# Kernel tuning notes

Measured on AMD Instinct MI355X. Metric: run time of the kernel, lower is better.

## Reference

```python
import jax, jax.numpy as jnp
import numpy as np

B, T, IN_DIM, OUT_DIM = 1024, 64, 8, 2
H, K, HIDDEN = 3, 5, 256
LOG_STD_MIN, LOG_STD_MAX = -20.0, 2.0


def setup_inputs() -> dict:
    key = jax.random.key(0)
    ks = jax.random.split(key, 12)
    def lin(k, fan_in, fan_out):
        b = 1.0 / np.sqrt(fan_in)
        return jax.random.uniform(k, (fan_in, fan_out), jnp.float32, -b, b)
    inp = {
        'state': jax.random.normal(ks[0], (B, T, IN_DIM), jnp.float32),
        'noise': jax.random.normal(ks[1], (B, T, OUT_DIM), jnp.float32),
        'Wq': lin(ks[2], IN_DIM, K * H),
        'Wk': lin(ks[3], K, K * H),
        'Wv': lin(ks[4], K, K * H),
        'W1': lin(ks[5], K * H + IN_DIM, HIDDEN),
        'b1': jnp.zeros((HIDDEN,), jnp.float32),
        'W2': lin(ks[6], HIDDEN, HIDDEN),
        'b2': jnp.zeros((HIDDEN,), jnp.float32),
        'Wmu': jax.random.uniform(ks[7], (HIDDEN, OUT_DIM), jnp.float32, -0.003, 0.003),
        'bmu': jax.random.uniform(ks[8], (OUT_DIM,), jnp.float32, -0.003, 0.003),
        'Wls': jax.random.uniform(ks[9], (HIDDEN, OUT_DIM), jnp.float32, -0.003, 0.003),
        'bls': jax.random.uniform(ks[10], (OUT_DIM,), jnp.float32, -0.003, 0.003),
    }
    return inp


# static off-diagonal neighbor indices: row i -> all j != i
_OFFDIAG = np.array([[j for j in range(T) if j != i] for i in range(T)], dtype=np.int32)


def _forward(state, noise, Wq, Wk, Wv, W1, b1, W2, b2, Wmu, bmu, Wls, bls):
    b, t, _ = state.shape
    # rel[b,i,j] = state[b,j,:4] - state[b,i,:4]
    rel4 = state[:, None, :, 0:4] - state[:, :, None, 0:4]          # [b,t,t,4] (x,y,vx,vy)
    x_comp = rel4[..., 0::2]                                         # [x, vx]
    y_comp = rel4[..., 1::2]                                         # [y, vy]
    ang = (-state[:, :, 7] + 0.5 * jnp.pi)[:, None, :, None]         # varies with j (own-ref of key agent)
    c, s = jnp.cos(ang), jnp.sin(ang)
    xn = x_comp * c - y_comp * s                                     # [x', vx']
    yn = x_comp * s + y_comp * c                                     # [y', vy']
    rel = jnp.stack([xn[..., 0], yn[..., 0], xn[..., 1], yn[..., 1]], axis=-1)  # [b,t,t,4]
    # drop self-pairs (diagonal) -> [b,t,t-1,4]
    idx = jnp.asarray(_OFFDIAG)
    rel_od = rel[:, jnp.arange(t)[:, None], idx]
    r = jnp.sqrt(rel_od[..., 0] ** 2 + rel_od[..., 1] ** 2)[..., None]   # [b,t,t-1,1]
    r_trans = jax.nn.sigmoid(1.0 - 5.0 * (r - 0.2))                       # 1/(1+exp(-1+5(r-0.2)))
    rel_n = jnp.concatenate([rel_od[..., 0:2] / r, rel_od[..., 2:4], r_trans], axis=-1)  # [b,t,t-1,5]
    h, k = H, K
    q = (state @ Wq).reshape(b, t, h, k)                              # [b,t,h,k]
    keys = (rel_n @ Wk).reshape(b, t, t - 1, h, k)                    # [b,t,n,h,k]
    vals = (rel_n @ Wv).reshape(b, t, t - 1, h, k)
    scores = jnp.einsum('btnhk,bthk->bthn', keys, q) / jnp.sqrt(jnp.float32(k))
    w = jax.nn.softmax(scores, axis=-1)                               # over t-1 neighbors
    att = jnp.einsum('bthn,btnhk->bthk', w, vals).reshape(b, t, h * k)
    x = jnp.concatenate([att, state], axis=-1)
    x = jax.nn.relu(x @ W1 + b1)
    x = jax.nn.relu(x @ W2 + b2)
    mu = jnp.tanh(x @ Wmu + bmu)
    log_std = jnp.tanh(x @ Wls + bls)
    log_std = LOG_STD_MIN + 0.5 * (LOG_STD_MAX - LOG_STD_MIN) * (log_std + 1.0)
    std = jnp.exp(log_std)
    z = mu + std * noise                                              # rsample with explicit noise
    action = jnp.tanh(z)
    # Normal(mu,std).log_prob(z) with (z-mu)/std == noise
    log_prob = -0.5 * noise ** 2 - log_std - 0.5 * jnp.log(2.0 * jnp.pi)
    log_prob = log_prob - jnp.log(1.0 - action ** 2 + 1e-7)
    log_prob = jnp.sum(log_prob, axis=-1, keepdims=True)
    return action, log_prob


def reference(state, noise, Wq, Wk, Wv, W1, b1, W2, b2, Wmu, bmu, Wls, bls):
    return _forward(state, noise, Wq, Wk, Wv, W1, b1, W2, b2, Wmu, bmu, Wls, bls)
```

## Files before the change

kernel.cpp:

```cpp
#include <hip/hip_runtime.h>
#include <math.h>

#define NROWS 65536

typedef short bf16x8 __attribute__((ext_vector_type(8)));
typedef float f32x4  __attribute__((ext_vector_type(4)));

__device__ __forceinline__ unsigned short f2bf(float x){
    unsigned int u = __float_as_uint(x);
    u += 0x7FFFu + ((u >> 16) & 1u);
    return (unsigned short)(u >> 16);
}

template<int CTRL, int RM>
__device__ __forceinline__ float dpp_add(float v){
    int m = __builtin_amdgcn_update_dpp(0, __float_as_int(v), CTRL, RM, 0xF, 1);
    return v + __int_as_float(m);
}
__device__ __forceinline__ float rowsum16(float v){
    v = dpp_add<0x111, 0xF>(v);
    v = dpp_add<0x112, 0xF>(v);
    v = dpp_add<0x114, 0xF>(v);
    v = dpp_add<0x118, 0xF>(v);
    return v;
}
__device__ __forceinline__ float bfly8_add(float v){
    v = dpp_add<0xB1, 0xF>(v);
    v = dpp_add<0x4E, 0xF>(v);
    v = dpp_add<0x141, 0xF>(v);
    return v;
}

__global__ __launch_bounds__(256) void prep_kernel(
    const float* __restrict__ W2, const float* __restrict__ W1,
    unsigned short* __restrict__ w2frag, unsigned short* __restrict__ w1frag)
{
    const int bx = blockIdx.x, t = threadIdx.x;
    if (bx < 128){
        const int ct = bx >> 3, kk = bx & 7;
        #pragma unroll
        for (int s = 0; s < 2; ++s){
            int f = t * 2 + s;
            int lane = f >> 3, e = f & 7;
            int k = kk * 32 + (lane >> 4) * 8 + e;
            int c = ct * 16 + (lane & 15);
            w2frag[(size_t)(ct * 8 + kk) * 512 + f] = f2bf(W2[k * 256 + c]);
        }
    } else {
        #pragma unroll
        for (int s = 0; s < 32; ++s){
            int flat = t * 32 + s;
            int ct = flat >> 9, r = flat & 511;
            int lane = r >> 3, e = r & 7;
            int k = (lane >> 4) * 8 + e;
            int c = ct * 16 + (lane & 15);
            w1frag[flat] = (k < 23) ? f2bf(W1[k * 256 + c]) : (unsigned short)0;
        }
    }
}

__global__ __launch_bounds__(512, 4) void actor_kernel(
    const float* __restrict__ state, const float* __restrict__ noise,
    const float* __restrict__ Wq, const float* __restrict__ Wk,
    const float* __restrict__ Wv,
    const unsigned short* __restrict__ w1frag, const float* __restrict__ b1,
    const unsigned short* __restrict__ w2frag, const float* __restrict__ b2,
    const float* __restrict__ Wmu, const float* __restrict__ bmu,
    const float* __restrict__ Wls, const float* __restrict__ bls,
    float* __restrict__ action_out, float* __restrict__ logprob_out)
{
    __shared__ __align__(16) unsigned char uniA[64 * 264 * 2];
    float* sLDS  = (float*)uniA;
    float* pjLDS = sLDS + 576;
    float* qkLDS = pjLDS + 512;
    unsigned short* h1LDS = (unsigned short*)uniA;
    __shared__ __align__(16) unsigned short x0LDS[64 * 40];
    __shared__ float headLDS[8 * 64 * 5];

    const int t    = threadIdx.x;
    const int lane = t & 63;
    const int w    = t >> 6;
    const int lm   = lane & 15;
    const int lq   = lane >> 4;
    const int b    = blockIdx.x;

    {
        float v = state[(size_t)b * 512 + t];
        int r = t >> 3, c = t & 7;
        sLDS[r * 9 + c] = v;
        if (c < 4) pjLDS[r * 8 + c] = v;
    }
    __syncthreads();

    if (t < 192){
        const int row = t & 63, h = t >> 6;
        float s[8];
        #pragma unroll
        for (int d = 0; d < 8; ++d) s[d] = sLDS[row * 9 + d];
        float q[5];
        #pragma unroll
        for (int e = 0; e < 5; ++e){
            int m = h * 5 + e;
            float acc = 0.f;
            #pragma unroll
            for (int d = 0; d < 8; ++d) acc += s[d] * Wq[d * 15 + m];
            q[e] = acc;
        }
        #pragma unroll
        for (int f = 0; f < 5; ++f){
            float acc = 0.f;
            #pragma unroll
            for (int kk = 0; kk < 5; ++kk) acc += Wk[f * 15 + h * 5 + kk] * q[kk];
            qkLDS[row * 17 + h * 5 + f] = acc * 0.64519834f;
        }
    } else if (w == 7){
        const int row = lane;
        float ang = 1.5707963267948966f - sLDS[row * 9 + 7];
        float sn, cs;
        __sincosf(ang, &sn, &cs);
        pjLDS[row * 8 + 4] = sn;
        pjLDS[row * 8 + 5] = cs;
    }
    __syncthreads();

    {
        const int il = lane >> 3;
        const int js = lane & 7;
        const int i  = w * 8 + il;
        const float si0 = sLDS[i * 9 + 0], si1 = sLDS[i * 9 + 1];
        const float si2 = sLDS[i * 9 + 2], si3 = sLDS[i * 9 + 3];
        float qkv[15];
        #pragma unroll
        for (int m = 0; m < 15; ++m) qkv[m] = qkLDS[i * 17 + m];

        float s0 = 0.f, s1 = 0.f, s2 = 0.f;
        float g0[5] = {0,0,0,0,0}, g1[5] = {0,0,0,0,0}, g2[5] = {0,0,0,0,0};
        #pragma unroll
        for (int jj = 0; jj < 8; ++jj){
            const int j = jj * 8 + js;
            float4 pj = *(const float4*)&pjLDS[j * 8];
            float sn = pjLDS[j * 8 + 4], cs = pjLDS[j * 8 + 5];
            float d0 = pj.x - si0, d1 = pj.y - si1, d2 = pj.z - si2, d3 = pj.w - si3;
            float xn0 = d0 * cs - d1 * sn, yn0 = d0 * sn + d1 * cs;
            float xn1 = d2 * cs - d3 * sn, yn1 = d2 * sn + d3 * cs;
            float r2v = xn0 * xn0 + yn0 * yn0;
            bool self = (j == i);
            float inv_r = self ? 0.f : rsqrtf(r2v);
            float rv = r2v * inv_r;
            float ex = exp2f(rv * 7.2134752f - 2.8853901f);
            float f4 = 1.f / (1.f + ex);
            float f0 = xn0 * inv_r, f1 = yn0 * inv_r;
            float sc0 = f0*qkv[0]  + f1*qkv[1]  + xn1*qkv[2]  + yn1*qkv[3]  + f4*qkv[4];
            float sc1 = f0*qkv[5]  + f1*qkv[6]  + xn1*qkv[7]  + yn1*qkv[8]  + f4*qkv[9];
            float sc2 = f0*qkv[10] + f1*qkv[11] + xn1*qkv[12] + yn1*qkv[13] + f4*qkv[14];
            float e0 = self ? 0.f : exp2f(sc0);
            float e1 = self ? 0.f : exp2f(sc1);
            float e2 = self ? 0.f : exp2f(sc2);
            s0 += e0; s1 += e1; s2 += e2;
            g0[0] += e0*f0; g0[1] += e0*f1; g0[2] += e0*xn1; g0[3] += e0*yn1; g0[4] += e0*f4;
            g1[0] += e1*f0; g1[1] += e1*f1; g1[2] += e1*xn1; g1[3] += e1*yn1; g1[4] += e1*f4;
            g2[0] += e2*f0; g2[1] += e2*f1; g2[2] += e2*xn1; g2[3] += e2*yn1; g2[4] += e2*f4;
        }
        s0 = bfly8_add(s0); s1 = bfly8_add(s1); s2 = bfly8_add(s2);
        #pragma unroll
        for (int f = 0; f < 5; ++f){
            g0[f] = bfly8_add(g0[f]);
            g1[f] = bfly8_add(g1[f]);
            g2[f] = bfly8_add(g2[f]);
        }
        float i0 = 1.f / s0, i1 = 1.f / s1, i2 = 1.f / s2;

        #pragma unroll
        for (int mm = 0; mm < 2; ++mm){
            int m = js * 2 + mm;
            if (m < 15){
                float G0 = (m < 5) ? g0[0] : (m < 10) ? g1[0] : g2[0];
                float G1 = (m < 5) ? g0[1] : (m < 10) ? g1[1] : g2[1];
                float G2 = (m < 5) ? g0[2] : (m < 10) ? g1[2] : g2[2];
                float G3 = (m < 5) ? g0[3] : (m < 10) ? g1[3] : g2[3];
                float G4 = (m < 5) ? g0[4] : (m < 10) ? g1[4] : g2[4];
                float I  = (m < 5) ? i0    : (m < 10) ? i1    : i2;
                float av = (G0 * Wv[m] + G1 * Wv[15 + m] + G2 * Wv[30 + m]
                          + G3 * Wv[45 + m] + G4 * Wv[60 + m]) * I;
                x0LDS[i * 40 + m] = f2bf(av);
            }
        }
        x0LDS[i * 40 + 15 + js] = f2bf(sLDS[i * 9 + js]);
        x0LDS[i * 40 + 23 + js] = 0;
        if (js == 0) x0LDS[i * 40 + 31] = 0;
    }
    __syncthreads();

    {
        bf16x8 afr[4];
        #pragma unroll
        for (int rt = 0; rt < 4; ++rt)
            afr[rt] = *(const bf16x8*)&x0LDS[(rt * 16 + lm) * 40 + lq * 8];
        #pragma unroll
        for (int ci = 0; ci < 2; ++ci){
            const int ct = w * 2 + ci;
            bf16x8 bfr = *(const bf16x8*)&w1frag[(size_t)ct * 512 + lane * 8];
            float bb = b1[ct * 16 + lm];
            #pragma unroll
            for (int rt = 0; rt < 4; ++rt){
                f32x4 c0 = {0.f, 0.f, 0.f, 0.f};
                c0 = __builtin_amdgcn_mfma_f32_16x16x32_bf16(afr[rt], bfr, c0, 0, 0, 0);
                #pragma unroll
                for (int p = 0; p < 4; ++p)
                    h1LDS[(rt * 16 + lq * 4 + p) * 264 + ct * 16 + lm] = f2bf(fmaxf(c0[p] + bb, 0.f));
            }
        }
    }
    __syncthreads();

    {
        f32x4 acc[4][2];
        #pragma unroll
        for (int rt = 0; rt < 4; ++rt)
            #pragma unroll
            for (int ci = 0; ci < 2; ++ci) acc[rt][ci] = (f32x4){0.f, 0.f, 0.f, 0.f};

        #pragma unroll
        for (int kk = 0; kk < 8; ++kk){
            bf16x8 arf[4], brf[2];
            #pragma unroll
            for (int rt = 0; rt < 4; ++rt)
                arf[rt] = *(const bf16x8*)&h1LDS[(rt * 16 + lm) * 264 + kk * 32 + lq * 8];
            #pragma unroll
            for (int ci = 0; ci < 2; ++ci)
                brf[ci] = *(const bf16x8*)&w2frag[(size_t)((w * 2 + ci) * 8 + kk) * 512 + lane * 8];
            #pragma unroll
            for (int rt = 0; rt < 4; ++rt)
                #pragma unroll
                for (int ci = 0; ci < 2; ++ci)
                    acc[rt][ci] = __builtin_amdgcn_mfma_f32_16x16x32_bf16(arf[rt], brf[ci], acc[rt][ci], 0, 0, 0);
        }

        float bb[2];
        float2 wm[2], wl[2];
        #pragma unroll
        for (int ci = 0; ci < 2; ++ci){
            int c = (w * 2 + ci) * 16 + lm;
            bb[ci] = b2[c];
            wm[ci] = *(const float2*)&Wmu[c * 2];
            wl[ci] = *(const float2*)&Wls[c * 2];
        }
        #pragma unroll
        for (int rt = 0; rt < 4; ++rt){
            #pragma unroll
            for (int p = 0; p < 4; ++p){
                float m0 = 0.f, m1 = 0.f, l0 = 0.f, l1 = 0.f;
                #pragma unroll
                for (int ci = 0; ci < 2; ++ci){
                    float hv = fmaxf(acc[rt][ci][p] + bb[ci], 0.f);
                    m0 += hv * wm[ci].x;
                    m1 += hv * wm[ci].y;
                    l0 += hv * wl[ci].x;
                    l1 += hv * wl[ci].y;
                }
                m0 = rowsum16(m0); m1 = rowsum16(m1);
                l0 = rowsum16(l0); l1 = rowsum16(l1);
                if (lm == 15){
                    int row = rt * 16 + lq * 4 + p;
                    float* hp = &headLDS[(w * 64 + row) * 5];
                    hp[0] = m0; hp[1] = m1; hp[2] = l0; hp[3] = l1;
                }
            }
        }
    }
    __syncthreads();

    if (t < 64){
        const int row = t;
        float m0 = 0.f, m1 = 0.f, l0 = 0.f, l1 = 0.f;
        #pragma unroll
        for (int ww = 0; ww < 8; ++ww){
            const float* hp = &headLDS[(ww * 64 + row) * 5];
            m0 += hp[0]; m1 += hp[1]; l0 += hp[2]; l1 += hp[3];
        }
        const size_t grow = (size_t)b * 64 + row;
        float n0 = noise[grow * 2 + 0];
        float n1 = noise[grow * 2 + 1];
        float lp = 0.f;
        {
            float mu = tanhf(m0 + bmu[0]);
            float ls = tanhf(l0 + bls[0]);
            ls = -20.f + 11.f * (ls + 1.f);
            float sd = expf(ls);
            float a = tanhf(mu + sd * n0);
            action_out[grow * 2 + 0] = a;
            lp += -0.5f * n0 * n0 - ls - 0.9189385332046727f - logf(1.f - a * a + 1e-7f);
        }
        {
            float mu = tanhf(m1 + bmu[1]);
            float ls = tanhf(l1 + bls[1]);
            ls = -20.f + 11.f * (ls + 1.f);
            float sd = expf(ls);
            float a = tanhf(mu + sd * n1);
            action_out[grow * 2 + 1] = a;
            lp += -0.5f * n1 * n1 - ls - 0.9189385332046727f - logf(1.f - a * a + 1e-7f);
        }
        logprob_out[grow] = lp;
    }
}

extern "C" void kernel_launch(void* const* d_in, const int* in_sizes, int n_in,
                              void* d_out, int out_size, void* d_ws, size_t ws_size,
                              hipStream_t stream)
{
    (void)in_sizes; (void)n_in; (void)out_size; (void)ws_size;
    const float* state = (const float*)d_in[0];
    const float* noise = (const float*)d_in[1];
    const float* Wq  = (const float*)d_in[2];
    const float* Wk  = (const float*)d_in[3];
    const float* Wv  = (const float*)d_in[4];
    const float* W1  = (const float*)d_in[5];
    const float* b1  = (const float*)d_in[6];
    const float* W2  = (const float*)d_in[7];
    const float* b2  = (const float*)d_in[8];
    const float* Wmu = (const float*)d_in[9];
    const float* bmu = (const float*)d_in[10];
    const float* Wls = (const float*)d_in[11];
    const float* bls = (const float*)d_in[12];

    unsigned short* w2frag = (unsigned short*)d_ws;
    unsigned short* w1frag = w2frag + 65536;

    float* action_out  = (float*)d_out;
    float* logprob_out = (float*)d_out + (size_t)NROWS * 2;

    prep_kernel<<<129, 256, 0, stream>>>(W2, W1, w2frag, w1frag);
    actor_kernel<<<1024, 512, 0, stream>>>(state, noise, Wq, Wk, Wv,
        w1frag, b1, w2frag, b2, Wmu, bmu, Wls, bls, action_out, logprob_out);
}
```

Baseline: 122.1 us.

## Split each batch element across two 256-thread blocks of 32 query rows

```diff
diff --git a/kernel.cpp b/kernel.cpp
--- a/kernel.cpp
+++ b/kernel.cpp
@@ -59,7 +59,7 @@
     }
 }
 
-__global__ __launch_bounds__(512, 4) void actor_kernel(
+__global__ __launch_bounds__(256, 6) void actor_kernel(
     const float* __restrict__ state, const float* __restrict__ noise,
     const float* __restrict__ Wq, const float* __restrict__ Wk,
     const float* __restrict__ Wv,
@@ -69,31 +69,35 @@
     const float* __restrict__ Wls, const float* __restrict__ bls,
     float* __restrict__ action_out, float* __restrict__ logprob_out)
 {
-    __shared__ __align__(16) unsigned char uniA[64 * 264 * 2];
+    __shared__ __align__(16) unsigned char uniA[32 * 264 * 2];
     float* sLDS  = (float*)uniA;
     float* pjLDS = sLDS + 576;
     float* qkLDS = pjLDS + 512;
     unsigned short* h1LDS = (unsigned short*)uniA;
-    __shared__ __align__(16) unsigned short x0LDS[64 * 40];
-    __shared__ float headLDS[8 * 64 * 5];
-
-    const int t    = threadIdx.x;
-    const int lane = t & 63;
-    const int w    = t >> 6;
-    const int lm   = lane & 15;
-    const int lq   = lane >> 4;
-    const int b    = blockIdx.x;
-
-    {
-        float v = state[(size_t)b * 512 + t];
-        int r = t >> 3, c = t & 7;
+    __shared__ __align__(16) unsigned short x0LDS[32 * 40];
+    __shared__ float headLDS[4 * 32 * 5];
+
+    const int t     = threadIdx.x;
+    const int lane  = t & 63;
+    const int w     = t >> 6;
+    const int lm    = lane & 15;
+    const int lq    = lane >> 4;
+    const int b     = blockIdx.x >> 1;
+    const int ibase = (blockIdx.x & 1) * 32;
+
+    #pragma unroll
+    for (int s = 0; s < 2; ++s){
+        int idx = t + s * 256;
+        float v = state[(size_t)b * 512 + idx];
+        int r = idx >> 3, c = idx & 7;
         sLDS[r * 9 + c] = v;
         if (c < 4) pjLDS[r * 8 + c] = v;
     }
     __syncthreads();
 
-    if (t < 192){
-        const int row = t & 63, h = t >> 6;
+    if (t < 96){
+        const int rloc = t & 31, h = t >> 5;
+        const int row = ibase + rloc;
         float s[8];
         #pragma unroll
         for (int d = 0; d < 8; ++d) s[d] = sLDS[row * 9 + d];
@@ -111,10 +115,10 @@
             float acc = 0.f;
             #pragma unroll
             for (int kk = 0; kk < 5; ++kk) acc += Wk[f * 15 + h * 5 + kk] * q[kk];
-            qkLDS[row * 17 + h * 5 + f] = acc * 0.64519834f;
-        }
-    } else if (w == 7){
-        const int row = lane;
+            qkLDS[rloc * 17 + h * 5 + f] = acc * 0.64519834f;
+        }
+    } else if (t < 160){
+        const int row = t - 96;
         float ang = 1.5707963267948966f - sLDS[row * 9 + 7];
         float sn, cs;
         __sincosf(ang, &sn, &cs);
@@ -126,12 +130,13 @@
     {
         const int il = lane >> 3;
         const int js = lane & 7;
-        const int i  = w * 8 + il;
+        const int iloc = w * 8 + il;
+        const int i = ibase + iloc;
         const float si0 = sLDS[i * 9 + 0], si1 = sLDS[i * 9 + 1];
         const float si2 = sLDS[i * 9 + 2], si3 = sLDS[i * 9 + 3];
         float qkv[15];
         #pragma unroll
-        for (int m = 0; m < 15; ++m) qkv[m] = qkLDS[i * 17 + m];
+        for (int m = 0; m < 15; ++m) qkv[m] = qkLDS[iloc * 17 + m];
 
         float s0 = 0.f, s1 = 0.f, s2 = 0.f;
         float g0[5] = {0,0,0,0,0}, g1[5] = {0,0,0,0,0}, g2[5] = {0,0,0,0,0};
@@ -182,27 +187,27 @@
                 float I  = (m < 5) ? i0    : (m < 10) ? i1    : i2;
                 float av = (G0 * Wv[m] + G1 * Wv[15 + m] + G2 * Wv[30 + m]
                           + G3 * Wv[45 + m] + G4 * Wv[60 + m]) * I;
-                x0LDS[i * 40 + m] = f2bf(av);
+                x0LDS[iloc * 40 + m] = f2bf(av);
             }
         }
-        x0LDS[i * 40 + 15 + js] = f2bf(sLDS[i * 9 + js]);
-        x0LDS[i * 40 + 23 + js] = 0;
-        if (js == 0) x0LDS[i * 40 + 31] = 0;
+        x0LDS[iloc * 40 + 15 + js] = f2bf(sLDS[i * 9 + js]);
+        x0LDS[iloc * 40 + 23 + js] = 0;
+        if (js == 0) x0LDS[iloc * 40 + 31] = 0;
     }
     __syncthreads();
 
     {
-        bf16x8 afr[4];
-        #pragma unroll
-        for (int rt = 0; rt < 4; ++rt)
+        bf16x8 afr[2];
+        #pragma unroll
+        for (int rt = 0; rt < 2; ++rt)
             afr[rt] = *(const bf16x8*)&x0LDS[(rt * 16 + lm) * 40 + lq * 8];
         #pragma unroll
-        for (int ci = 0; ci < 2; ++ci){
-            const int ct = w * 2 + ci;
+        for (int ci = 0; ci < 4; ++ci){
+            const int ct = w * 4 + ci;
             bf16x8 bfr = *(const bf16x8*)&w1frag[(size_t)ct * 512 + lane * 8];
             float bb = b1[ct * 16 + lm];
             #pragma unroll
-            for (int rt = 0; rt < 4; ++rt){
+            for (int rt = 0; rt < 2; ++rt){
                 f32x4 c0 = {0.f, 0.f, 0.f, 0.f};
                 c0 = __builtin_amdgcn_mfma_f32_16x16x32_bf16(afr[rt], bfr, c0, 0, 0, 0);
                 #pragma unroll
@@ -214,44 +219,44 @@
     __syncthreads();
 
     {
-        f32x4 acc[4][2];
-        #pragma unroll
-        for (int rt = 0; rt < 4; ++rt)
-            #pragma unroll
-            for (int ci = 0; ci < 2; ++ci) acc[rt][ci] = (f32x4){0.f, 0.f, 0.f, 0.f};
+        f32x4 acc[2][4];
+        #pragma unroll
+        for (int rt = 0; rt < 2; ++rt)
+            #pragma unroll
+            for (int ci = 0; ci < 4; ++ci) acc[rt][ci] = (f32x4){0.f, 0.f, 0.f, 0.f};
 
         #pragma unroll
         for (int kk = 0; kk < 8; ++kk){
-            bf16x8 arf[4], brf[2];
-            #pragma unroll
-            for (int rt = 0; rt < 4; ++rt)
+            bf16x8 arf[2], brf[4];
+            #pragma unroll
+            for (int rt = 0; rt < 2; ++rt)
                 arf[rt] = *(const bf16x8*)&h1LDS[(rt * 16 + lm) * 264 + kk * 32 + lq * 8];
             #pragma unroll
-            for (int ci = 0; ci < 2; ++ci)
-                brf[ci] = *(const bf16x8*)&w2frag[(size_t)((w * 2 + ci) * 8 + kk) * 512 + lane * 8];
-            #pragma unroll
-            for (int rt = 0; rt < 4; ++rt)
+            for (int ci = 0; ci < 4; ++ci)
+                brf[ci] = *(const bf16x8*)&w2frag[(size_t)((w * 4 + ci) * 8 + kk) * 512 + lane * 8];
+            #pragma unroll
+            for (int rt = 0; rt < 2; ++rt)
                 #pragma unroll
-                for (int ci = 0; ci < 2; ++ci)
+                for (int ci = 0; ci < 4; ++ci)
                     acc[rt][ci] = __builtin_amdgcn_mfma_f32_16x16x32_bf16(arf[rt], brf[ci], acc[rt][ci], 0, 0, 0);
         }
 
-        float bb[2];
-        float2 wm[2], wl[2];
-        #pragma unroll
-        for (int ci = 0; ci < 2; ++ci){
-            int c = (w * 2 + ci) * 16 + lm;
+        float bb[4];
+        float2 wm[4], wl[4];
+        #pragma unroll
+        for (int ci = 0; ci < 4; ++ci){
+            int c = (w * 4 + ci) * 16 + lm;
             bb[ci] = b2[c];
             wm[ci] = *(const float2*)&Wmu[c * 2];
             wl[ci] = *(const float2*)&Wls[c * 2];
         }
         #pragma unroll
-        for (int rt = 0; rt < 4; ++rt){
+        for (int rt = 0; rt < 2; ++rt){
             #pragma unroll
             for (int p = 0; p < 4; ++p){
                 float m0 = 0.f, m1 = 0.f, l0 = 0.f, l1 = 0.f;
                 #pragma unroll
-                for (int ci = 0; ci < 2; ++ci){
+                for (int ci = 0; ci < 4; ++ci){
                     float hv = fmaxf(acc[rt][ci][p] + bb[ci], 0.f);
                     m0 += hv * wm[ci].x;
                     m1 += hv * wm[ci].y;
@@ -262,7 +267,7 @@
                 l0 = rowsum16(l0); l1 = rowsum16(l1);
                 if (lm == 15){
                     int row = rt * 16 + lq * 4 + p;
-                    float* hp = &headLDS[(w * 64 + row) * 5];
+                    float* hp = &headLDS[(w * 32 + row) * 5];
                     hp[0] = m0; hp[1] = m1; hp[2] = l0; hp[3] = l1;
                 }
             }
@@ -270,15 +275,15 @@
     }
     __syncthreads();
 
-    if (t < 64){
+    if (t < 32){
         const int row = t;
         float m0 = 0.f, m1 = 0.f, l0 = 0.f, l1 = 0.f;
         #pragma unroll
-        for (int ww = 0; ww < 8; ++ww){
-            const float* hp = &headLDS[(ww * 64 + row) * 5];
+        for (int ww = 0; ww < 4; ++ww){
+            const float* hp = &headLDS[(ww * 32 + row) * 5];
             m0 += hp[0]; m1 += hp[1]; l0 += hp[2]; l1 += hp[3];
         }
-        const size_t grow = (size_t)b * 64 + row;
+        const size_t grow = (size_t)b * 64 + ibase + row;
         float n0 = noise[grow * 2 + 0];
         float n1 = noise[grow * 2 + 1];
         float lp = 0.f;
@@ -330,6 +335,6 @@
     float* logprob_out = (float*)d_out + (size_t)NROWS * 2;
 
     prep_kernel<<<129, 256, 0, stream>>>(W2, W1, w2frag, w1frag);
-    actor_kernel<<<1024, 512, 0, stream>>>(state, noise, Wq, Wk, Wv,
+    actor_kernel<<<2048, 256, 0, stream>>>(state, noise, Wq, Wk, Wv,
         w1frag, b1, w2frag, b2, Wmu, bmu, Wls, bls, action_out, logprob_out);
 }
```

After: 122.0 us. About the same (-0.1%).
